# Kernel tuning notes

Hardware: AMD Instinct MI355X
Metric: run time of the kernel (lower is better)

Reference implementation:

```python
import jax, jax.numpy as jnp
import numpy as np

EPS = 1e-12  # tf.linalg.l2_normalize epsilon

def l2norm(x, axis):
    sq = jnp.sum(x * x, axis=axis, keepdims=True)
    return x * jax.lax.rsqrt(jnp.maximum(sq, EPS))

def setup_inputs() -> dict:
    key = jax.random.key(0)
    k1, k2, k3, k4 = jax.random.split(key, 4)
    B, S, D = 32, 2048, 1024
    X = jax.random.normal(k1, (B, S, D), dtype=jnp.float32)
    lengths = jax.random.randint(k2, (B,), 1, S + 1).astype(jnp.int32)
    W_global = jax.random.normal(k3, (D, D), dtype=jnp.float32) / np.sqrt(D)
    W_local = jax.random.normal(k4, (D, D), dtype=jnp.float32) / np.sqrt(D)
    return {"X": X, "lengths": lengths, "W_global": W_global, "W_local": W_local}

def reference(X, lengths, W_global, W_local):
    B, S, D = X.shape
    # ragged -> dense with mask: token s valid iff s < lengths[b]
    mask = (jnp.arange(S)[None, :] < lengths[:, None]).astype(X.dtype)  # [B,S]
    Xm = X * mask[:, :, None]
    # global projection of sequence-sum, l2-normalized per example
    gp = l2norm(jnp.sum(Xm, axis=1) @ W_global, axis=1)  # [B,D]
    # per-token local projection, l2-normalized per token
    lp = l2norm(jnp.einsum('bsd,de->bse', Xm, W_local), axis=2)  # [B,S,D]
    # dot-product attention of local projections against global vector
    attention = jnp.einsum('bsd,bd->bs', lp, gp) * mask  # [B,S]
    # attention-weighted sum over the (ragged) sequence
    return jnp.einsum('bs,bsd->bd', attention, Xm)  # [B,D]
```

## Files before the change

### kernel.cpp

```cpp
#include <hip/hip_runtime.h>

#define NB 32
#define NS 2048
#define ND 1024

typedef unsigned short u16;
typedef unsigned int u32;
typedef __attribute__((ext_vector_type(8))) short bf16x8;
typedef __attribute__((ext_vector_type(4))) float f32x4;

__device__ __forceinline__ u16 f2bf(float f) {
    u32 u = __float_as_uint(f);
    u32 r = u + 0x7fffu + ((u >> 16) & 1u);
    return (u16)(r >> 16);
}

template <bool DO_STASH>
__global__ void k_prep(const float* __restrict__ X, const int* __restrict__ len,
                       float* __restrict__ sumX, u16* __restrict__ stash) {
    int b = blockIdx.x >> 5, c = blockIdx.x & 31;
    int L = len[b];
    int s0 = c * 64;
    if (s0 >= L) return;
    int n = min(64, L - s0);
    int t = threadIdx.x;
    const float4* base = (const float4*)(X + (size_t)b * NS * ND + (size_t)s0 * ND) + t;
    u16* tb = stash + ((size_t)blockIdx.x << 16)
            + (size_t)(t >> 3) * 2048 + (((t >> 1) & 3) << 7) + ((t & 1) << 2);
    float4 acc = {0.f, 0.f, 0.f, 0.f};
    for (int i = 0; i < n; ++i) {
        float4 x = base[i * (ND / 4)];
        acc.x += x.x; acc.y += x.y; acc.z += x.z; acc.w += x.w;
        if constexpr (DO_STASH) {
            u32 lo = (u32)f2bf(x.x) | ((u32)f2bf(x.y) << 16);
            u32 hi = (u32)f2bf(x.z) | ((u32)f2bf(x.w) << 16);
            *(uint2*)(tb + (i >> 4) * 512 + (i & 15) * 8) = make_uint2(lo, hi);
        }
    }
    if constexpr (DO_STASH) {
        for (int i = n; i < 64; ++i)
            *(uint2*)(tb + (i >> 4) * 512 + (i & 15) * 8) = make_uint2(0u, 0u);
    }
    float* o = sumX + b * ND + t * 4;
    atomicAdd(o + 0, acc.x); atomicAdd(o + 1, acc.y);
    atomicAdd(o + 2, acc.z); atomicAdd(o + 3, acc.w);
}

__global__ void k_pack(const float* __restrict__ Wl, u16* __restrict__ pack) {
    int t = threadIdx.x;
    int f = blockIdx.x * 4 + (t >> 6);
    int lane = t & 63;
    int j = f & 3, kk = (f >> 2) & 31, nc = f >> 7;
    int n = nc * 64 + j * 16 + (lane & 15);
    int k0 = kk * 32 + ((lane >> 4) << 3);
    u16 tmp[8];
    #pragma unroll
    for (int e = 0; e < 8; ++e)
        tmp[e] = f2bf(Wl[(size_t)(k0 + e) * ND + n]);
    *(uint4*)(pack + (size_t)f * 512 + lane * 8) = *(const uint4*)tmp;
}

__global__ void k_gproj(const float* __restrict__ sumX, const float* __restrict__ Wg,
                        float* __restrict__ yg) {
    __shared__ float sx[32][64];
    int t = threadIdx.x;
    int eb = blockIdx.x & 15, db = blockIdx.x >> 4;
    int e = eb * 64 + (t & 63);
    int bg = t >> 6;
    float acc[8] = {0.f,0.f,0.f,0.f,0.f,0.f,0.f,0.f};
    for (int d0 = db * 128; d0 < db * 128 + 128; d0 += 64) {
        __syncthreads();
        #pragma unroll
        for (int j = 0; j < 8; ++j) {
            int idx = t + j * 256;
            sx[idx >> 6][idx & 63] = sumX[(idx >> 6) * ND + d0 + (idx & 63)];
        }
        __syncthreads();
        for (int dd = 0; dd < 64; ++dd) {
            float wv = Wg[(size_t)(d0 + dd) * ND + e];
            #pragma unroll
            for (int j = 0; j < 8; ++j) acc[j] += wv * sx[bg * 8 + j][dd];
        }
    }
    #pragma unroll
    for (int j = 0; j < 8; ++j) atomicAdd(&yg[(bg * 8 + j) * ND + e], acc[j]);
}

__global__ void k_gnorm(const float* __restrict__ yg, float* __restrict__ gp) {
    int b = blockIdx.x, t = threadIdx.x;
    float4 y = ((const float4*)(yg + (size_t)b * ND))[t];
    float ss = y.x * y.x + y.y * y.y + y.z * y.z + y.w * y.w;
    #pragma unroll
    for (int o = 32; o; o >>= 1) ss += __shfl_down(ss, o);
    __shared__ float wsum[4];
    if ((t & 63) == 0) wsum[t >> 6] = ss;
    __syncthreads();
    float tot = wsum[0] + wsum[1] + wsum[2] + wsum[3];
    float sc = 1.f / sqrtf(fmaxf(tot, 1e-12f));
    float4 g = {y.x * sc, y.y * sc, y.z * sc, y.w * sc};
    ((float4*)(gp + (size_t)b * ND))[t] = g;
}

template <bool STASH>
__global__ __launch_bounds__(256, 3) void k_main(
    const float* __restrict__ X, const int* __restrict__ len,
    const u16* __restrict__ stash, const u16* __restrict__ pack,
    const float* __restrict__ gp, float* __restrict__ out) {
    __shared__ float gp_s[1024];
    __shared__ float norm2_s[4][64];
    __shared__ float dot_s[4][64];
    __shared__ float att_s[64];

    int b = blockIdx.x >> 5;
    int tile = blockIdx.x & 31;
    int L = len[b];
    int s0 = tile * 64;
    if (s0 >= L) return;
    int valid = min(64, L - s0);
    int t = threadIdx.x;
    int lane = t & 63, w = t >> 6;

    for (int jj = t; jj < 1024; jj += 256) gp_s[jj] = gp[b * ND + jj];
    ((float*)norm2_s)[t] = 0.f;
    ((float*)dot_s)[t] = 0.f;
    __syncthreads();

    const u16* ta = stash + ((size_t)blockIdx.x << 16) + lane * 8;
    const float* Xb = X + (size_t)b * NS * ND + (size_t)s0 * ND;

    for (int q = 0; q < 4; ++q) {
        int nc = w + q * 4;
        const u16* pb = pack + (size_t)nc * 65536 + lane * 8;
        f32x4 acc[4][4];
        #pragma unroll
        for (int rb = 0; rb < 4; ++rb)
            #pragma unroll
            for (int j = 0; j < 4; ++j) acc[rb][j] = (f32x4){0.f, 0.f, 0.f, 0.f};

        #pragma unroll 2
        for (int kk = 0; kk < 32; ++kk) {
            bf16x8 a[4], bb[4];
            if constexpr (STASH) {
                #pragma unroll
                for (int rb = 0; rb < 4; ++rb)
                    a[rb] = *(const bf16x8*)(ta + (kk * 4 + rb) * 512);
            } else {
                int kb = kk * 32 + ((lane >> 4) << 3);
                #pragma unroll
                for (int rb = 0; rb < 4; ++rb) {
                    int row = (rb << 4) + (lane & 15);
                    bf16x8 av = {0,0,0,0,0,0,0,0};
                    if (row < valid) {
                        float4 x0 = *(const float4*)(Xb + (size_t)row * ND + kb);
                        float4 x1 = *(const float4*)(Xb + (size_t)row * ND + kb + 4);
                        av[0] = (short)f2bf(x0.x); av[1] = (short)f2bf(x0.y);
                        av[2] = (short)f2bf(x0.z); av[3] = (short)f2bf(x0.w);
                        av[4] = (short)f2bf(x1.x); av[5] = (short)f2bf(x1.y);
                        av[6] = (short)f2bf(x1.z); av[7] = (short)f2bf(x1.w);
                    }
                    a[rb] = av;
                }
            }
            #pragma unroll
            for (int j = 0; j < 4; ++j)
                bb[j] = *(const bf16x8*)(pb + (kk * 4 + j) * 512);
            #pragma unroll
            for (int j = 0; j < 4; ++j)
                #pragma unroll
                for (int rb = 0; rb < 4; ++rb)
                    acc[rb][j] = __builtin_amdgcn_mfma_f32_16x16x32_bf16(a[rb], bb[j], acc[rb][j], 0, 0, 0);
        }
        float gpv[4];
        #pragma unroll
        for (int j = 0; j < 4; ++j) gpv[j] = gp_s[nc * 64 + j * 16 + (lane & 15)];
        #pragma unroll
        for (int rb = 0; rb < 4; ++rb) {
            #pragma unroll
            for (int reg = 0; reg < 4; ++reg) {
                float s = 0.f, d = 0.f;
                #pragma unroll
                for (int j = 0; j < 4; ++j) {
                    float y = acc[rb][j][reg];
                    s += y * y;
                    d += y * gpv[j];
                }
                s += __shfl_xor(s, 1); d += __shfl_xor(d, 1);
                s += __shfl_xor(s, 2); d += __shfl_xor(d, 2);
                s += __shfl_xor(s, 4); d += __shfl_xor(d, 4);
                s += __shfl_xor(s, 8); d += __shfl_xor(d, 8);
                if ((lane & 15) == 0) {
                    int row = (rb << 4) + ((lane >> 4) << 2) + reg;
                    norm2_s[w][row] += s;
                    dot_s[w][row] += d;
                }
            }
        }
    }
    __syncthreads();

    if (t < 64) {
        float n2 = norm2_s[0][t] + norm2_s[1][t] + norm2_s[2][t] + norm2_s[3][t];
        float dp = dot_s[0][t] + dot_s[1][t] + dot_s[2][t] + dot_s[3][t];
        att_s[t] = dp / sqrtf(fmaxf(n2, 1e-12f));
    }
    __syncthreads();

    {
        float4 acc4 = {0.f, 0.f, 0.f, 0.f};
        #pragma unroll 4
        for (int i = 0; i < valid; ++i) {
            float a = att_s[i];
            float4 x = ((const float4*)(Xb + (size_t)i * ND))[t];
            acc4.x += a * x.x; acc4.y += a * x.y; acc4.z += a * x.z; acc4.w += a * x.w;
        }
        float* o = out + b * ND + t * 4;
        atomicAdd(o + 0, acc4.x); atomicAdd(o + 1, acc4.y);
        atomicAdd(o + 2, acc4.z); atomicAdd(o + 3, acc4.w);
    }
}

extern "C" void kernel_launch(void* const* d_in, const int* in_sizes, int n_in,
                              void* d_out, int out_size, void* d_ws, size_t ws_size,
                              hipStream_t stream) {
    (void)in_sizes; (void)n_in; (void)out_size;
    const float* X  = (const float*)d_in[0];
    const int* len  = (const int*)d_in[1];
    const float* Wg = (const float*)d_in[2];
    const float* Wl = (const float*)d_in[3];
    float* out = (float*)d_out;

    char* ws = (char*)d_ws;
    float* sumX = (float*)(ws + 0);
    float* yg   = (float*)(ws + 131072);
    float* gp   = (float*)(ws + 262144);
    u16*   pack = (u16*)(ws + 393216);
    u16*   stash= (u16*)(ws + 2490368);
    const size_t need = 2490368ull + (size_t)NB * 32 * 131072ull;
    int use_stash = ws_size >= need;

    hipMemsetAsync(sumX, 0, 2 * NB * ND * sizeof(float), stream);
    hipMemsetAsync(out, 0, NB * ND * sizeof(float), stream);

    if (use_stash)
        k_prep<true> <<<NB * 32, 256, 0, stream>>>(X, len, sumX, stash);
    else
        k_prep<false><<<NB * 32, 256, 0, stream>>>(X, len, sumX, stash);
    k_pack <<<512, 256, 0, stream>>>(Wl, pack);
    k_gproj<<<128, 256, 0, stream>>>(sumX, Wg, yg);
    k_gnorm<<<NB, 256, 0, stream>>>(yg, gp);
    if (use_stash)
        k_main<true> <<<NB * 32, 256, 0, stream>>>(X, len, stash, pack, gp, out);
    else
        k_main<false><<<NB * 32, 256, 0, stream>>>(X, len, stash, pack, gp, out);
}
```

Before: 605.0 us.

## Split MFMA K-loop across blocks, replace atomics with partials, tile W pack

The main projection kernel is split into two blocks per 64-token tile, each covering half of the K dimension. Per-row norm and dot partials are written to workspace, and a new k_out kernel combines them and does the attention-weighted sum over X. Sequence-sum and global-projection atomics become per-chunk partial buffers reduced by new kernels, and the Wl bf16 packing now goes through an LDS tile so global reads are coalesced. This doubles the grid for better CU occupancy and removes atomic contention, at the cost of extra launches, a second pass over X, and more workspace that may disable the stash path.

```diff
diff --git a/kernel.cpp b/kernel.cpp
--- a/kernel.cpp
+++ b/kernel.cpp
@@ -17,7 +17,7 @@
 
 template <bool DO_STASH>
 __global__ void k_prep(const float* __restrict__ X, const int* __restrict__ len,
-                       float* __restrict__ sumX, u16* __restrict__ stash) {
+                       float* __restrict__ partial, u16* __restrict__ stash) {
     int b = blockIdx.x >> 5, c = blockIdx.x & 31;
     int L = len[b];
     int s0 = c * 64;
@@ -41,27 +41,47 @@
         for (int i = n; i < 64; ++i)
             *(uint2*)(tb + (i >> 4) * 512 + (i & 15) * 8) = make_uint2(0u, 0u);
     }
-    float* o = sumX + b * ND + t * 4;
-    atomicAdd(o + 0, acc.x); atomicAdd(o + 1, acc.y);
-    atomicAdd(o + 2, acc.z); atomicAdd(o + 3, acc.w);
+    *(float4*)(partial + ((size_t)(c * NB + b)) * ND + t * 4) = acc;
+}
+
+__global__ void k_reduce(const float* __restrict__ partial, float* __restrict__ sumX) {
+    int b = blockIdx.x >> 2, dq = blockIdx.x & 3;
+    int d = dq * 256 + threadIdx.x;
+    float s = 0.f;
+    #pragma unroll
+    for (int c = 0; c < 32; ++c) s += partial[((size_t)(c * NB + b)) * ND + d];
+    sumX[b * ND + d] = s;
 }
 
 __global__ void k_pack(const float* __restrict__ Wl, u16* __restrict__ pack) {
-    int t = threadIdx.x;
-    int f = blockIdx.x * 4 + (t >> 6);
-    int lane = t & 63;
-    int j = f & 3, kk = (f >> 2) & 31, nc = f >> 7;
-    int n = nc * 64 + j * 16 + (lane & 15);
-    int k0 = kk * 32 + ((lane >> 4) << 3);
-    u16 tmp[8];
-    #pragma unroll
-    for (int e = 0; e < 8; ++e)
-        tmp[e] = f2bf(Wl[(size_t)(k0 + e) * ND + n]);
-    *(uint4*)(pack + (size_t)f * 512 + lane * 8) = *(const uint4*)tmp;
+    __shared__ float tile[64][65];
+    int t = threadIdx.x;
+    int kt = blockIdx.x >> 4, nt = blockIdx.x & 15;
+    int k0 = kt * 64, n0 = nt * 64;
+    #pragma unroll
+    for (int rep = 0; rep < 4; ++rep) {
+        int idx4 = t + rep * 256;
+        int r = idx4 >> 4, c4 = idx4 & 15;
+        float4 w4 = *(const float4*)(Wl + (size_t)(k0 + r) * ND + n0 + c4 * 4);
+        tile[r][c4 * 4 + 0] = w4.x; tile[r][c4 * 4 + 1] = w4.y;
+        tile[r][c4 * 4 + 2] = w4.z; tile[r][c4 * 4 + 3] = w4.w;
+    }
+    __syncthreads();
+    u32* p32 = (u32*)pack;
+    int l = t >> 2, epair = (t & 3) * 2;
+    #pragma unroll
+    for (int f = 0; f < 8; ++f) {
+        int kk2 = f >> 2, j = f & 3;
+        int kloc = kk2 * 32 + (l >> 4) * 8 + epair;
+        int nloc = j * 16 + (l & 15);
+        u32 v = (u32)f2bf(tile[kloc][nloc]) | ((u32)f2bf(tile[kloc + 1][nloc]) << 16);
+        int fg = nt * 128 + (kt * 2 + kk2) * 4 + j;
+        p32[(size_t)fg * 256 + t] = v;
+    }
 }
 
 __global__ void k_gproj(const float* __restrict__ sumX, const float* __restrict__ Wg,
-                        float* __restrict__ yg) {
+                        float* __restrict__ ygp) {
     __shared__ float sx[32][64];
     int t = threadIdx.x;
     int eb = blockIdx.x & 15, db = blockIdx.x >> 4;
@@ -83,12 +103,18 @@
         }
     }
     #pragma unroll
-    for (int j = 0; j < 8; ++j) atomicAdd(&yg[(bg * 8 + j) * ND + e], acc[j]);
-}
-
-__global__ void k_gnorm(const float* __restrict__ yg, float* __restrict__ gp) {
+    for (int j = 0; j < 8; ++j)
+        ygp[((size_t)(db * NB) + bg * 8 + j) * ND + e] = acc[j];
+}
+
+__global__ void k_gnorm(const float* __restrict__ ygp, float* __restrict__ gp) {
     int b = blockIdx.x, t = threadIdx.x;
-    float4 y = ((const float4*)(yg + (size_t)b * ND))[t];
+    float4 y = {0.f, 0.f, 0.f, 0.f};
+    #pragma unroll
+    for (int db = 0; db < 8; ++db) {
+        float4 p = ((const float4*)(ygp + (size_t)(db * NB + b) * ND))[t];
+        y.x += p.x; y.y += p.y; y.z += p.z; y.w += p.w;
+    }
     float ss = y.x * y.x + y.y * y.y + y.z * y.z + y.w * y.w;
     #pragma unroll
     for (int o = 32; o; o >>= 1) ss += __shfl_down(ss, o);
@@ -102,30 +128,31 @@
 }
 
 template <bool STASH>
-__global__ __launch_bounds__(256, 3) void k_main(
+__global__ __launch_bounds__(256, 3) void k_mfma(
     const float* __restrict__ X, const int* __restrict__ len,
     const u16* __restrict__ stash, const u16* __restrict__ pack,
-    const float* __restrict__ gp, float* __restrict__ out) {
+    const float* __restrict__ gp, float* __restrict__ norm2p, float* __restrict__ dotp) {
     __shared__ float gp_s[1024];
     __shared__ float norm2_s[4][64];
     __shared__ float dot_s[4][64];
-    __shared__ float att_s[64];
-
-    int b = blockIdx.x >> 5;
-    int tile = blockIdx.x & 31;
+
+    int b = blockIdx.x >> 6;
+    int tile = (blockIdx.x >> 1) & 31;
+    int kh = blockIdx.x & 1;
     int L = len[b];
     int s0 = tile * 64;
     if (s0 >= L) return;
     int valid = min(64, L - s0);
     int t = threadIdx.x;
     int lane = t & 63, w = t >> 6;
+    int kh16 = kh * 16;
 
     for (int jj = t; jj < 1024; jj += 256) gp_s[jj] = gp[b * ND + jj];
     ((float*)norm2_s)[t] = 0.f;
     ((float*)dot_s)[t] = 0.f;
     __syncthreads();
 
-    const u16* ta = stash + ((size_t)blockIdx.x << 16) + lane * 8;
+    const u16* ta = stash + ((size_t)(b * 32 + tile) << 16) + lane * 8;
     const float* Xb = X + (size_t)b * NS * ND + (size_t)s0 * ND;
 
     for (int q = 0; q < 4; ++q) {
@@ -138,7 +165,7 @@
             for (int j = 0; j < 4; ++j) acc[rb][j] = (f32x4){0.f, 0.f, 0.f, 0.f};
 
         #pragma unroll 2
-        for (int kk = 0; kk < 32; ++kk) {
+        for (int kk = kh16; kk < kh16 + 16; ++kk) {
             bf16x8 a[4], bb[4];
             if constexpr (STASH) {
                 #pragma unroll
@@ -197,26 +224,41 @@
         }
     }
     __syncthreads();
-
     if (t < 64) {
-        float n2 = norm2_s[0][t] + norm2_s[1][t] + norm2_s[2][t] + norm2_s[3][t];
-        float dp = dot_s[0][t] + dot_s[1][t] + dot_s[2][t] + dot_s[3][t];
+        int idx = (b * 32 + tile) * 64 + t;
+        norm2p[kh * 65536 + idx] = norm2_s[0][t] + norm2_s[1][t] + norm2_s[2][t] + norm2_s[3][t];
+        dotp[kh * 65536 + idx]   = dot_s[0][t] + dot_s[1][t] + dot_s[2][t] + dot_s[3][t];
+    }
+}
+
+__global__ void k_out(const float* __restrict__ X, const int* __restrict__ len,
+                      const float* __restrict__ norm2p, const float* __restrict__ dotp,
+                      float* __restrict__ out) {
+    __shared__ float att_s[64];
+    int b = blockIdx.x >> 5, tile = blockIdx.x & 31;
+    int L = len[b];
+    int s0 = tile * 64;
+    if (s0 >= L) return;
+    int valid = min(64, L - s0);
+    int t = threadIdx.x;
+    if (t < 64) {
+        int idx = (b * 32 + tile) * 64 + t;
+        float n2 = norm2p[idx] + norm2p[65536 + idx];
+        float dp = dotp[idx] + dotp[65536 + idx];
         att_s[t] = dp / sqrtf(fmaxf(n2, 1e-12f));
     }
     __syncthreads();
-
-    {
-        float4 acc4 = {0.f, 0.f, 0.f, 0.f};
-        #pragma unroll 4
-        for (int i = 0; i < valid; ++i) {
-            float a = att_s[i];
-            float4 x = ((const float4*)(Xb + (size_t)i * ND))[t];
-            acc4.x += a * x.x; acc4.y += a * x.y; acc4.z += a * x.z; acc4.w += a * x.w;
-        }
-        float* o = out + b * ND + t * 4;
-        atomicAdd(o + 0, acc4.x); atomicAdd(o + 1, acc4.y);
-        atomicAdd(o + 2, acc4.z); atomicAdd(o + 3, acc4.w);
-    }
+    const float* Xb = X + (size_t)b * NS * ND + (size_t)s0 * ND;
+    float4 acc4 = {0.f, 0.f, 0.f, 0.f};
+    #pragma unroll 4
+    for (int i = 0; i < valid; ++i) {
+        float a = att_s[i];
+        float4 x = ((const float4*)(Xb + (size_t)i * ND))[t];
+        acc4.x += a * x.x; acc4.y += a * x.y; acc4.z += a * x.z; acc4.w += a * x.w;
+    }
+    float* o = out + b * ND + t * 4;
+    atomicAdd(o + 0, acc4.x); atomicAdd(o + 1, acc4.y);
+    atomicAdd(o + 2, acc4.z); atomicAdd(o + 3, acc4.w);
 }
 
 extern "C" void kernel_launch(void* const* d_in, const int* in_sizes, int n_in,
@@ -230,26 +272,31 @@
     float* out = (float*)d_out;
 
     char* ws = (char*)d_ws;
-    float* sumX = (float*)(ws + 0);
-    float* yg   = (float*)(ws + 131072);
-    float* gp   = (float*)(ws + 262144);
-    u16*   pack = (u16*)(ws + 393216);
-    u16*   stash= (u16*)(ws + 2490368);
-    const size_t need = 2490368ull + (size_t)NB * 32 * 131072ull;
+    float* partial = (float*)(ws + 0);
+    float* sumX    = (float*)(ws + 4194304);
+    float* ygp     = (float*)(ws + 4325376);
+    float* gp      = (float*)(ws + 5373952);
+    u16*   pack    = (u16*)(ws + 5505024);
+    float* norm2p  = (float*)(ws + 7602176);
+    float* dotp    = (float*)(ws + 8126464);
+    u16*   stash   = (u16*)(ws + 8650752);
+    const size_t need = 8650752ull + (size_t)NB * 32 * 131072ull;
     int use_stash = ws_size >= need;
 
-    hipMemsetAsync(sumX, 0, 2 * NB * ND * sizeof(float), stream);
+    hipMemsetAsync(partial, 0, 4194304, stream);
     hipMemsetAsync(out, 0, NB * ND * sizeof(float), stream);
 
     if (use_stash)
-        k_prep<true> <<<NB * 32, 256, 0, stream>>>(X, len, sumX, stash);
+        k_prep<true> <<<NB * 32, 256, 0, stream>>>(X, len, partial, stash);
     else
-        k_prep<false><<<NB * 32, 256, 0, stream>>>(X, len, sumX, stash);
-    k_pack <<<512, 256, 0, stream>>>(Wl, pack);
-    k_gproj<<<128, 256, 0, stream>>>(sumX, Wg, yg);
-    k_gnorm<<<NB, 256, 0, stream>>>(yg, gp);
+        k_prep<false><<<NB * 32, 256, 0, stream>>>(X, len, partial, stash);
+    k_reduce<<<128, 256, 0, stream>>>(partial, sumX);
+    k_pack  <<<256, 256, 0, stream>>>(Wl, pack);
+    k_gproj <<<128, 256, 0, stream>>>(sumX, Wg, ygp);
+    k_gnorm <<<NB, 256, 0, stream>>>(ygp, gp);
     if (use_stash)
-        k_main<true> <<<NB * 32, 256, 0, stream>>>(X, len, stash, pack, gp, out);
+        k_mfma<true> <<<NB * 32 * 2, 256, 0, stream>>>(X, len, stash, pack, gp, norm2p, dotp);
     else
-        k_main<false><<<NB * 32, 256, 0, stream>>>(X, len, stash, pack, gp, out);
-}
+        k_mfma<false><<<NB * 32 * 2, 256, 0, stream>>>(X, len, stash, pack, gp, norm2p, dotp);
+    k_out  <<<NB * 32, 256, 0, stream>>>(X, len, norm2p, dotp, out);
+}
```

Measured after the change: 608.5 us. About the same (+0.6%).
